# Optimization experiments

Hardware: AMD Instinct MI355X
Metric: run time of the kernel (lower is better)

## Reference

```python
import jax, jax.numpy as jnp
import numpy as np

B, N, IN_DIM, H, D = 4, 2048, 128, 4, 64
NEG_SLOPE = 0.2
MASK_VAL = -1e9


def setup_inputs() -> dict:
    key = jax.random.key(0)
    k1, k2, k3, k4, k5 = jax.random.split(key, 5)
    x = jax.random.normal(k1, (B, N, IN_DIM), dtype=jnp.float32)
    adj = jax.random.randint(k2, (N, N), 0, 2, dtype=jnp.int32)
    W = jax.random.normal(k3, (H * D, IN_DIM), dtype=jnp.float32) * 0.05
    att_src = jax.random.normal(k4, (1, H, D), dtype=jnp.float32) * 0.05
    att_dst = jax.random.normal(k5, (1, H, D), dtype=jnp.float32) * 0.05
    return {"x": x, "adj": adj, "W": W, "att_src": att_src, "att_dst": att_dst}


def reference(x, adj, W, att_src, att_dst):
    # linear (no bias), torch layout: y = x @ W.T  -> [B,N,H*D]
    h = jnp.einsum('bni,oi->bno', x, W).reshape(B, N, H, D).transpose(0, 2, 1, 3)  # [B,H,N,D]
    e_src = jnp.einsum('bhnd,hd->bhn', h, att_src[0])  # [B,H,N]
    e_dst = jnp.einsum('bhnd,hd->bhn', h, att_dst[0])  # [B,H,N]
    # additive score: e[b,h,i,j] = leaky_relu(e_src[b,h,i] + e_dst[b,h,j])
    e = jax.nn.leaky_relu(e_src[..., :, None] + e_dst[..., None, :], NEG_SLOPE)  # [B,H,N,N]
    e = jnp.where(adj[None, None] <= 0, MASK_VAL, e)
    attn = jax.nn.softmax(e, axis=-1)  # dropout inactive (inference)
    out = jnp.einsum('bhij,bhjd->bhid', attn, h)  # [B,H,N,D]
    return out.transpose(0, 2, 1, 3).reshape(B, N, H * D)  # concat heads
```

## Files before the change

kernel.cpp:

```cpp
#include <hip/hip_runtime.h>


#define NDIM 2048
#define NEG_SLOPE 0.2f
#define LOG2E 1.4426950408889634f

typedef __bf16 bf16x8 __attribute__((ext_vector_type(8)));
typedef __bf16 bf16x4 __attribute__((ext_vector_type(4)));
typedef float  f32x4  __attribute__((ext_vector_type(4)));

#define LP 136
#define HP 72

__global__ __launch_bounds__(256) void adj_pack(const int* __restrict__ adj,
                                                unsigned* __restrict__ bits) {
    const int t = threadIdx.x;
    const int q = blockIdx.x * 256 + t;
    int4 a = ((const int4*)adj)[q];
    unsigned nib = (unsigned)(a.x > 0) | ((unsigned)(a.y > 0) << 1) |
                   ((unsigned)(a.z > 0) << 2) | ((unsigned)(a.w > 0) << 3);
    unsigned v = nib << ((t & 7) * 4);
    v |= __shfl_xor(v, 1, 64);
    v |= __shfl_xor(v, 2, 64);
    v |= __shfl_xor(v, 4, 64);
    if ((t & 7) == 0) bits[q >> 3] = v;
}

__global__ __launch_bounds__(256) void gat_linear(
    const float* __restrict__ x, const float* __restrict__ W,
    const float* __restrict__ att_src, const float* __restrict__ att_dst,
    __bf16* __restrict__ h_t, float* __restrict__ es_ws, float* __restrict__ ed_ws)
{
    const int t    = threadIdx.x;
    const int head = blockIdx.x & 3;
    const int n0g  = (blockIdx.x >> 2) * 64;
    const int b    = n0g >> 11;
    const int n0   = n0g & (NDIM - 1);
    const int bh   = b * 4 + head;

    __shared__ __align__(16) __bf16 Wl[64][LP];
    __shared__ __align__(16) __bf16 Xl[64][LP];

    #pragma unroll
    for (int i = 0; i < 8; ++i) {
        int idx = t + i * 256;
        int r = idx >> 5, c4 = idx & 31;
        float4 wv = *((const float4*)(W + (size_t)(head * 64 + r) * 128) + c4);
        bf16x4 bv;
        bv[0] = (__bf16)wv.x; bv[1] = (__bf16)wv.y; bv[2] = (__bf16)wv.z; bv[3] = (__bf16)wv.w;
        *(bf16x4*)&Wl[r][c4 * 4] = bv;
    }
    #pragma unroll
    for (int i = 0; i < 8; ++i) {
        int idx = t + i * 256;
        int r = idx >> 5, c4 = idx & 31;
        float4 xv = *((const float4*)(x + (size_t)(n0g + r) * 128) + c4);
        bf16x4 bv;
        bv[0] = (__bf16)xv.x; bv[1] = (__bf16)xv.y; bv[2] = (__bf16)xv.z; bv[3] = (__bf16)xv.w;
        *(bf16x4*)&Xl[r][c4 * 4] = bv;
    }
    __syncthreads();

    const int lane = t & 63, w = t >> 6;
    const int m = lane & 15, q4 = lane >> 4;

    bf16x8 bfr[4];
    #pragma unroll
    for (int ks = 0; ks < 4; ++ks)
        bfr[ks] = *(const bf16x8*)&Xl[w * 16 + m][ks * 32 + q4 * 8];

    f32x4 acc[4];
    #pragma unroll
    for (int c = 0; c < 4; ++c) acc[c] = (f32x4){0.f, 0.f, 0.f, 0.f};

    #pragma unroll
    for (int ct = 0; ct < 4; ++ct) {
        #pragma unroll
        for (int ks = 0; ks < 4; ++ks) {
            bf16x8 afr = *(const bf16x8*)&Wl[ct * 16 + m][ks * 32 + q4 * 8];
            acc[ct] = __builtin_amdgcn_mfma_f32_16x16x32_bf16(afr, bfr[ks], acc[ct], 0, 0, 0);
        }
    }

    const int nloc = n0 + w * 16 + m;
    float esA = 0.f, edA = 0.f;
    #pragma unroll
    for (int ct = 0; ct < 4; ++ct) {
        float4 aS = *(const float4*)(att_src + head * 64 + ct * 16 + q4 * 4);
        float4 aD = *(const float4*)(att_dst + head * 64 + ct * 16 + q4 * 4);
        #pragma unroll
        for (int r = 0; r < 4; ++r) {
            float v = acc[ct][r];
            int   d = ct * 16 + q4 * 4 + r;
            h_t[(size_t)(bh * 64 + d) * NDIM + nloc] = (__bf16)v;
            esA += v * ((const float*)&aS)[r];
            edA += v * ((const float*)&aD)[r];
        }
    }
    esA += __shfl_xor(esA, 16, 64); esA += __shfl_xor(esA, 32, 64);
    edA += __shfl_xor(edA, 16, 64); edA += __shfl_xor(edA, 32, 64);
    if (lane < 16) {
        es_ws[bh * NDIM + nloc] = esA;
        ed_ws[bh * NDIM + nloc] = edA;
    }
}

__global__ __launch_bounds__(256) void gat_attn(
    const unsigned long long* __restrict__ bits, const __bf16* __restrict__ h_t,
    const float* __restrict__ es_ws, const float* __restrict__ ed_ws,
    float* __restrict__ out)
{
    const int blk = blockIdx.x;
    const int bh  = blk & 15;
    const int i0  = (blk >> 4) * 64;
    const int t   = threadIdx.x;
    const int lane = t & 63, w = t >> 6;
    const int m = lane & 15, q4 = lane >> 4;
    const int il = t >> 2;
    const int ch = t & 3;

    __shared__ __align__(16) __bf16 Hl[2][64][HP];
    __shared__ float eds[NDIM];

    #pragma unroll
    for (int k = 0; k < 2; ++k) {
        int idx = t + k * 256;
        float4 v = ((const float4*)(ed_ws + bh * NDIM))[idx];
        v.x *= LOG2E; v.y *= LOG2E; v.z *= LOG2E; v.w *= LOG2E;
        ((float4*)eds)[idx] = v;
    }
    const float es2 = es_ws[bh * NDIM + i0 + w * 16 + m] * LOG2E;
    const unsigned long long* brow = bits + (size_t)(i0 + w * 16 + m) * 32;

    const __bf16* hbase = h_t + (size_t)(bh * 64 + il) * NDIM + ch * 16;
    {
        bf16x8 c0 = *(const bf16x8*)hbase;
        bf16x8 c1 = *(const bf16x8*)(hbase + 8);
        *(bf16x8*)&Hl[0][il][ch * 16]     = c0;
        *(bf16x8*)&Hl[0][il][ch * 16 + 8] = c1;
    }
    __syncthreads();

    f32x4 acc[4];
    #pragma unroll
    for (int c = 0; c < 4; ++c) acc[c] = (f32x4){0.f, 0.f, 0.f, 0.f};
    float lacc = 0.f;

    for (int itj = 0; itj < 32; ++itj) {
        const int buf = itj & 1;
        const bool hn = itj < 31;
        bf16x8 n0v, n1v;
        if (hn) {
            const __bf16* gp = hbase + (itj + 1) * 64;
            n0v = *(const bf16x8*)gp;
            n1v = *(const bf16x8*)(gp + 8);
        }

        const unsigned long long bw = brow[itj];
        const int j0 = itj * 64;
        bf16x8 af[2];
        #pragma unroll
        for (int ks = 0; ks < 2; ++ks) {
            float e[8];
            *(float4*)&e[0] = *(const float4*)&eds[j0 + ks * 32 + q4 * 8];
            *(float4*)&e[4] = *(const float4*)&eds[j0 + ks * 32 + q4 * 8 + 4];
            unsigned bm = (unsigned)(bw >> (ks * 32 + q4 * 8)) & 0xFFu;
            #pragma unroll
            for (int jj = 0; jj < 8; ++jj) {
                float s = es2 + e[jj];
                s = fmaxf(s, NEG_SLOPE * s);
                s = ((bm >> jj) & 1u) ? s : -10000.0f;
                float p = __builtin_amdgcn_exp2f(s);
                lacc += p;
                af[ks][jj] = (__bf16)p;
            }
        }

        #pragma unroll
        for (int ks = 0; ks < 2; ++ks) {
            #pragma unroll
            for (int ct = 0; ct < 4; ++ct) {
                bf16x8 bfr = *(const bf16x8*)&Hl[buf][ct * 16 + m][ks * 32 + q4 * 8];
                acc[ct] = __builtin_amdgcn_mfma_f32_16x16x32_bf16(af[ks], bfr, acc[ct], 0, 0, 0);
            }
        }

        if (hn) {
            *(bf16x8*)&Hl[buf ^ 1][il][ch * 16]     = n0v;
            *(bf16x8*)&Hl[buf ^ 1][il][ch * 16 + 8] = n1v;
        }
        __syncthreads();
    }

    lacc += __shfl_xor(lacc, 16, 64);
    lacc += __shfl_xor(lacc, 32, 64);
    const float inv = 1.f / lacc;
    float invr[4];
    #pragma unroll
    for (int r = 0; r < 4; ++r) invr[r] = __shfl(inv, q4 * 4 + r, 64);

    const int b = bh >> 2, head = bh & 3;
    float* ob = out + ((size_t)(b * NDIM + i0 + w * 16)) * 256 + head * 64;
    #pragma unroll
    for (int ct = 0; ct < 4; ++ct) {
        #pragma unroll
        for (int r = 0; r < 4; ++r) {
            ob[(size_t)(q4 * 4 + r) * 256 + ct * 16 + m] = acc[ct][r] * invr[r];
        }
    }
}

extern "C" void kernel_launch(void* const* d_in, const int* in_sizes, int n_in,
                              void* d_out, int out_size, void* d_ws, size_t ws_size,
                              hipStream_t stream) {
    const float* x       = (const float*)d_in[0];
    const int*   adj     = (const int*)d_in[1];
    const float* W       = (const float*)d_in[2];
    const float* att_src = (const float*)d_in[3];
    const float* att_dst = (const float*)d_in[4];
    float* out = (float*)d_out;

    __bf16*   h_t   = (__bf16*)d_ws;
    float*    es_ws = (float*)((char*)d_ws + (size_t)4 * 1024 * 1024);
    float*    ed_ws = es_ws + 16 * NDIM;
    unsigned* bitsp = (unsigned*)(ed_ws + 16 * NDIM);

    adj_pack<<<NDIM * NDIM / 4 / 256, 256, 0, stream>>>(adj, bitsp);
    gat_linear<<<512, 256, 0, stream>>>(x, W, att_src, att_dst, h_t, es_ws, ed_ws);
    gat_attn<<<512, 256, 0, stream>>>((const unsigned long long*)bitsp, h_t, es_ws, ed_ws, out);
}
```

Baseline: 108.6 us.

## Use direct global-to-LDS async loads, swizzled H tile, and MFMA row sums

The attention kernel now stages H tiles with global_load_lds straight into an unpadded, XOR-swizzled LDS buffer instead of loading through registers. It prefetches ed values and adjacency words into registers one step ahead rather than staging ed in shared memory. The softmax denominator is accumulated with an extra MFMA against a vector of ones, and LOG2E scaling moves into the linear kernel. The aim is to cut VGPR/VALU work and LDS traffic and to overlap memory with compute, at the cost of one extra MFMA per k-step and a more involved swizzle.

```diff
diff --git a/kernel.cpp b/kernel.cpp
--- a/kernel.cpp
+++ b/kernel.cpp
@@ -10,7 +10,12 @@
 typedef float  f32x4  __attribute__((ext_vector_type(4)));
 
 #define LP 136
-#define HP 72
+
+__device__ static inline void load_lds16(const void* g, void* l) {
+    __builtin_amdgcn_global_load_lds(
+        (const __attribute__((address_space(1))) unsigned*)g,
+        (__attribute__((address_space(3))) unsigned*)l, 16, 0, 0);
+}
 
 __global__ __launch_bounds__(256) void adj_pack(const int* __restrict__ adj,
                                                 unsigned* __restrict__ bits) {
@@ -100,8 +105,8 @@
     esA += __shfl_xor(esA, 16, 64); esA += __shfl_xor(esA, 32, 64);
     edA += __shfl_xor(edA, 16, 64); edA += __shfl_xor(edA, 32, 64);
     if (lane < 16) {
-        es_ws[bh * NDIM + nloc] = esA;
-        ed_ws[bh * NDIM + nloc] = edA;
+        es_ws[bh * NDIM + nloc] = esA * LOG2E;
+        ed_ws[bh * NDIM + nloc] = edA * LOG2E;
     }
 }
 
@@ -116,88 +121,89 @@
     const int t   = threadIdx.x;
     const int lane = t & 63, w = t >> 6;
     const int m = lane & 15, q4 = lane >> 4;
-    const int il = t >> 2;
-    const int ch = t & 3;
-
-    __shared__ __align__(16) __bf16 Hl[2][64][HP];
-    __shared__ float eds[NDIM];
-
-    #pragma unroll
-    for (int k = 0; k < 2; ++k) {
-        int idx = t + k * 256;
-        float4 v = ((const float4*)(ed_ws + bh * NDIM))[idx];
-        v.x *= LOG2E; v.y *= LOG2E; v.z *= LOG2E; v.w *= LOG2E;
-        ((float4*)eds)[idx] = v;
-    }
-    const float es2 = es_ws[bh * NDIM + i0 + w * 16 + m] * LOG2E;
+
+    __shared__ __align__(16) __bf16 Hl[2][64][64];
+
+    const int r0 = w * 16 + (lane >> 3);
+    const int r1 = r0 + 8;
+    const int c8 = lane & 7;
+    const __bf16* g0 = h_t + ((size_t)(bh * 64 + r0)) * NDIM + ((c8 ^ (r0 & 7)) * 8);
+    const __bf16* g1 = h_t + ((size_t)(bh * 64 + r1)) * NDIM + ((c8 ^ (r1 & 7)) * 8);
+    __bf16* l0a = &Hl[0][r0][c8 * 8];
+    __bf16* l0b = &Hl[0][r1][c8 * 8];
+    __bf16* l1a = &Hl[1][r0][c8 * 8];
+    __bf16* l1b = &Hl[1][r1][c8 * 8];
+
+    const float es2 = es_ws[bh * NDIM + i0 + w * 16 + m];
     const unsigned long long* brow = bits + (size_t)(i0 + w * 16 + m) * 32;
-
-    const __bf16* hbase = h_t + (size_t)(bh * 64 + il) * NDIM + ch * 16;
-    {
-        bf16x8 c0 = *(const bf16x8*)hbase;
-        bf16x8 c1 = *(const bf16x8*)(hbase + 8);
-        *(bf16x8*)&Hl[0][il][ch * 16]     = c0;
-        *(bf16x8*)&Hl[0][il][ch * 16 + 8] = c1;
-    }
+    const float* edp = ed_ws + bh * NDIM + q4 * 8;
+
+    load_lds16(g0, l0a);
+    load_lds16(g1, l0b);
+    float eb[2][16];
+    unsigned long long bwb[2];
+    #pragma unroll
+    for (int g = 0; g < 4; ++g)
+        *(float4*)&eb[0][g * 4] = *(const float4*)(edp + (g >> 1) * 32 + (g & 1) * 4);
+    bwb[0] = brow[0];
+
+    f32x4 acc[4], accl;
+    #pragma unroll
+    for (int c = 0; c < 4; ++c) acc[c] = (f32x4){0.f, 0.f, 0.f, 0.f};
+    accl = (f32x4){0.f, 0.f, 0.f, 0.f};
+    bf16x8 ones;
+    #pragma unroll
+    for (int jj = 0; jj < 8; ++jj) ones[jj] = (__bf16)1.0f;
+    const int sw = m & 7;
+
     __syncthreads();
 
-    f32x4 acc[4];
-    #pragma unroll
-    for (int c = 0; c < 4; ++c) acc[c] = (f32x4){0.f, 0.f, 0.f, 0.f};
-    float lacc = 0.f;
-
-    for (int itj = 0; itj < 32; ++itj) {
-        const int buf = itj & 1;
-        const bool hn = itj < 31;
-        bf16x8 n0v, n1v;
-        if (hn) {
-            const __bf16* gp = hbase + (itj + 1) * 64;
-            n0v = *(const bf16x8*)gp;
-            n1v = *(const bf16x8*)(gp + 8);
-        }
-
-        const unsigned long long bw = brow[itj];
-        const int j0 = itj * 64;
-        bf16x8 af[2];
-        #pragma unroll
-        for (int ks = 0; ks < 2; ++ks) {
-            float e[8];
-            *(float4*)&e[0] = *(const float4*)&eds[j0 + ks * 32 + q4 * 8];
-            *(float4*)&e[4] = *(const float4*)&eds[j0 + ks * 32 + q4 * 8 + 4];
-            unsigned bm = (unsigned)(bw >> (ks * 32 + q4 * 8)) & 0xFFu;
-            #pragma unroll
-            for (int jj = 0; jj < 8; ++jj) {
-                float s = es2 + e[jj];
-                s = fmaxf(s, NEG_SLOPE * s);
-                s = ((bm >> jj) & 1u) ? s : -10000.0f;
-                float p = __builtin_amdgcn_exp2f(s);
-                lacc += p;
-                af[ks][jj] = (__bf16)p;
-            }
-        }
-
-        #pragma unroll
-        for (int ks = 0; ks < 2; ++ks) {
-            #pragma unroll
-            for (int ct = 0; ct < 4; ++ct) {
-                bf16x8 bfr = *(const bf16x8*)&Hl[buf][ct * 16 + m][ks * 32 + q4 * 8];
-                acc[ct] = __builtin_amdgcn_mfma_f32_16x16x32_bf16(af[ks], bfr, acc[ct], 0, 0, 0);
-            }
-        }
-
-        if (hn) {
-            *(bf16x8*)&Hl[buf ^ 1][il][ch * 16]     = n0v;
-            *(bf16x8*)&Hl[buf ^ 1][il][ch * 16 + 8] = n1v;
-        }
-        __syncthreads();
-    }
-
-    lacc += __shfl_xor(lacc, 16, 64);
-    lacc += __shfl_xor(lacc, 32, 64);
-    const float inv = 1.f / lacc;
+#define STEP(ITJ, P)                                                            \
+    {                                                                           \
+        const int itj = (ITJ);                                                  \
+        if (itj < 31) {                                                         \
+            load_lds16(g0 + (itj + 1) * 64, (P) ? l0a : l1a);                   \
+            load_lds16(g1 + (itj + 1) * 64, (P) ? l0b : l1b);                   \
+            const float* ep = edp + (itj + 1) * 64;                             \
+            _Pragma("unroll")                                                   \
+            for (int g = 0; g < 4; ++g)                                         \
+                *(float4*)&eb[(P) ^ 1][g * 4] =                                 \
+                    *(const float4*)(ep + (g >> 1) * 32 + (g & 1) * 4);         \
+            bwb[(P) ^ 1] = brow[itj + 1];                                       \
+        }                                                                       \
+        bf16x8 af[2];                                                           \
+        _Pragma("unroll")                                                       \
+        for (int ks = 0; ks < 2; ++ks) {                                        \
+            unsigned bm = (unsigned)(bwb[P] >> (ks * 32 + q4 * 8)) & 0xFFu;     \
+            _Pragma("unroll")                                                   \
+            for (int jj = 0; jj < 8; ++jj) {                                    \
+                float s = es2 + eb[P][ks * 8 + jj];                             \
+                s = fmaxf(s, NEG_SLOPE * s);                                    \
+                s = ((bm >> jj) & 1u) ? s : -10000.0f;                          \
+                af[ks][jj] = (__bf16)__builtin_amdgcn_exp2f(s);                 \
+            }                                                                   \
+        }                                                                       \
+        _Pragma("unroll")                                                       \
+        for (int ks = 0; ks < 2; ++ks) {                                        \
+            accl = __builtin_amdgcn_mfma_f32_16x16x32_bf16(af[ks], ones, accl, 0, 0, 0); \
+            _Pragma("unroll")                                                   \
+            for (int ct = 0; ct < 4; ++ct) {                                    \
+                bf16x8 bfr = *(const bf16x8*)&Hl[P][ct * 16 + m][(((ks * 4 + q4) ^ sw)) * 8]; \
+                acc[ct] = __builtin_amdgcn_mfma_f32_16x16x32_bf16(af[ks], bfr, acc[ct], 0, 0, 0); \
+            }                                                                   \
+        }                                                                       \
+        __syncthreads();                                                        \
+    }
+
+    for (int it2 = 0; it2 < 16; ++it2) {
+        STEP(it2 * 2, 0);
+        STEP(it2 * 2 + 1, 1);
+    }
+#undef STEP
+
     float invr[4];
     #pragma unroll
-    for (int r = 0; r < 4; ++r) invr[r] = __shfl(inv, q4 * 4 + r, 64);
+    for (int r = 0; r < 4; ++r) invr[r] = 1.f / accl[r];
 
     const int b = bh >> 2, head = bh & 3;
     float* ob = out + ((size_t)(b * NDIM + i0 + w * 16)) * 256 + head * 64;
```

After: 108.2 us, median of 2. Within noise of the previous version (-0.3%).
